# Performance work log

Measured on AMD Instinct MI355X. Metric: run time of the kernel, lower is better.

## Reference

```python
import jax, jax.numpy as jnp
import numpy as np

N_NODES = 50000
N_EDGES = 600000
IN_FEATS = 128
HIDDEN = 256
OUT_FEATS = 64


def setup_inputs() -> dict:
    key = jax.random.key(0)
    ks = jax.random.split(key, 12)
    inv = lambda n: 1.0 / np.sqrt(n)
    return {
        "x": jax.random.normal(ks[0], (N_NODES, IN_FEATS), dtype=jnp.float32),
        "edge_index": jax.random.randint(ks[1], (2, N_EDGES), 0, N_NODES, dtype=jnp.int64),
        "W_sage": jax.random.normal(ks[2], (IN_FEATS, IN_FEATS), dtype=jnp.float32) * inv(IN_FEATS),
        "W1a": jax.random.normal(ks[3], (IN_FEATS, HIDDEN), dtype=jnp.float32) * inv(IN_FEATS),
        "b1a": jax.random.normal(ks[4], (HIDDEN,), dtype=jnp.float32) * 0.01,
        "W1b": jax.random.normal(ks[5], (HIDDEN, OUT_FEATS), dtype=jnp.float32) * inv(HIDDEN),
        "b1b": jax.random.normal(ks[6], (OUT_FEATS,), dtype=jnp.float32) * 0.01,
        "W2a": jax.random.normal(ks[7], (IN_FEATS, HIDDEN), dtype=jnp.float32) * inv(IN_FEATS),
        "b2a": jax.random.normal(ks[8], (HIDDEN,), dtype=jnp.float32) * 0.01,
        "W2b": jax.random.normal(ks[9], (HIDDEN, OUT_FEATS), dtype=jnp.float32) * inv(HIDDEN),
        "b2b": jax.random.normal(ks[10], (OUT_FEATS,), dtype=jnp.float32) * 0.01,
    }


def reference(x, edge_index, W_sage, W1a, b1a, W1b, b1b, W2a, b2a, W2b, b2b):
    n = x.shape[0]
    src, dst = edge_index[0], edge_index[1]
    # SAGEConv mean aggregation: mean over incoming neighbor (source) features at each target node
    summed = jax.ops.segment_sum(x[src], dst, num_segments=n)          # [N, in]
    deg = jax.ops.segment_sum(jnp.ones_like(src, dtype=x.dtype), dst, num_segments=n)
    mean = summed / jnp.maximum(deg, 1.0)[:, None]                     # nodes w/o neighbors -> 0
    x_1hop = mean @ W_sage                                             # lin_l, no root, no bias
    # dual MLP branches (dropout is identity in eval mode)
    out1 = jax.nn.relu(x @ W1a + b1a) @ W1b + b1b
    out2 = jax.nn.relu(x_1hop @ W2a + b2a) @ W2b + b2b
    return out1 + out2
```

## Files before the change

### kernel.cpp

```cpp
#include <hip/hip_runtime.h>

#define N_NODES 50000
#define N_PAD   50048
#define N_EDGES 600000
#define IN_F 128
#define HID 256
#define OUT_F 64
#define ROWS 16
#define SLOTS 56
#define NBLK (N_PAD / ROWS)
#define EPT 4

typedef __attribute__((ext_vector_type(8))) short bf16x8;
typedef __attribute__((ext_vector_type(4))) float f32x4;

__device__ inline short f2bf(float f) {
    unsigned u = __builtin_bit_cast(unsigned, f);
    u += 0x7fffu + ((u >> 16) & 1u);
    return (short)(u >> 16);
}
__device__ inline float bflo(unsigned u) { return __builtin_bit_cast(float, u << 16); }
__device__ inline float bfhi(unsigned u) { return __builtin_bit_cast(float, u & 0xffff0000u); }

__global__ __launch_bounds__(256) void build_kernel(
    const int* __restrict__ ei, int* __restrict__ cursor,
    unsigned short* __restrict__ esrc)
{
    int t0 = blockIdx.x * (256 * EPT) + threadIdx.x;
    int src[EPT], dst[EPT], p[EPT];
    bool v[EPT];
    #pragma unroll
    for (int i = 0; i < EPT; ++i) {
        int e = t0 + i * 256;
        v[i] = e < N_EDGES;
        int ee = v[i] ? e : 0;
        src[i] = ei[ee];
        dst[i] = ei[N_EDGES + ee];
    }
    #pragma unroll
    for (int i = 0; i < EPT; ++i)
        p[i] = v[i] ? atomicAdd(&cursor[dst[i]], 1) : SLOTS;
    #pragma unroll
    for (int i = 0; i < EPT; ++i)
        if (v[i] && p[i] < SLOTS)
            esrc[(size_t)dst[i] * SLOTS + p[i]] = (unsigned short)src[i];
}

__global__ __launch_bounds__(256) void prep_kernel(
    const float* __restrict__ x, short* __restrict__ xb,
    const float* __restrict__ Wsg, const float* __restrict__ W2a,
    const float* __restrict__ W1a, const float* __restrict__ W1b,
    const float* __restrict__ W2b,
    short* __restrict__ F1a, short* __restrict__ F1b,
    short* __restrict__ Fc,  short* __restrict__ F2b)
{
    const int bid = blockIdx.x, t = threadIdx.x;
    if (bid < 3125) {
        int i = bid * 256 + t;
        float4 a0 = *reinterpret_cast<const float4*>(x + (size_t)i * 8);
        float4 a1 = *reinterpret_cast<const float4*>(x + (size_t)i * 8 + 4);
        bf16x8 v;
        v[0] = f2bf(a0.x); v[1] = f2bf(a0.y); v[2] = f2bf(a0.z); v[3] = f2bf(a0.w);
        v[4] = f2bf(a1.x); v[5] = f2bf(a1.y); v[6] = f2bf(a1.z); v[7] = f2bf(a1.w);
        *reinterpret_cast<bf16x8*>(xb + (size_t)i * 8) = v;
        return;
    }
    int cid = (bid - 3125) * 256 + t;
    if (cid >= 6144 && cid < 10240) {
        int c = cid - 6144;
        int lane = c & 63, rem = c >> 6;
        int ks = rem & 3, nt = rem >> 2;
        int col = nt * 16 + (lane & 15);
        int k0 = ks * 32 + (lane >> 4) * 8;
        float acc[8] = {0.f, 0.f, 0.f, 0.f, 0.f, 0.f, 0.f, 0.f};
        for (int m0 = 0; m0 < 128; m0 += 8) {
            float wcol[8];
            #pragma unroll
            for (int mm = 0; mm < 8; ++mm)
                wcol[mm] = W2a[(size_t)(m0 + mm) * HID + col];
            #pragma unroll
            for (int j = 0; j < 8; ++j) {
                #pragma unroll
                for (int mm = 0; mm < 8; ++mm)
                    acc[j] = fmaf(Wsg[(size_t)(k0 + j) * IN_F + m0 + mm], wcol[mm], acc[j]);
            }
        }
        bf16x8 v;
        #pragma unroll
        for (int j = 0; j < 8; ++j) v[j] = f2bf(acc[j]);
        *reinterpret_cast<bf16x8*>(Fc + (size_t)c * 8) = v;
    } else {
        const float* src; short* dst; int N, KST, base;
        if      (cid < 4096)  { src = W1a; dst = F1a; N = 256; KST = 4; base = 0; }
        else if (cid < 6144)  { src = W1b; dst = F1b; N = 64;  KST = 8; base = 4096; }
        else                  { src = W2b; dst = F2b; N = 64;  KST = 8; base = 10240; }
        int c = cid - base;
        int lane = c & 63;
        int rem = c >> 6;
        int ks = rem % KST;
        int nt = rem / KST;
        int col = nt * 16 + (lane & 15);
        int k0 = ks * 32 + (lane >> 4) * 8;
        bf16x8 v;
        #pragma unroll
        for (int j = 0; j < 8; ++j)
            v[j] = f2bf(src[(size_t)(k0 + j) * N + col]);
        *reinterpret_cast<bf16x8*>(dst + (size_t)c * 8) = v;
    }
}

__device__ inline bf16x8 afrag_lds128(const short* S, int lane, int ks) {
    int row = lane & 15, g = lane >> 4;
    int chunk = (ks * 4 + g) ^ row;
    return *reinterpret_cast<const bf16x8*>(
        reinterpret_cast<const char*>(S) + row * 256 + chunk * 16);
}
__device__ inline bf16x8 afrag_lds256(const short* S, int lane, int ks) {
    int row = lane & 15, g = lane >> 4;
    int chunk = (ks * 4 + g) ^ row;
    return *reinterpret_cast<const bf16x8*>(
        reinterpret_cast<const char*>(S) + row * 512 + chunk * 16);
}

__device__ inline void stage1_relu(const bf16x8 afr[4], short* Hs,
                                   const short* __restrict__ Waf,
                                   const float* __restrict__ ba,
                                   int w, int lane)
{
    const int row16 = lane & 15, g = lane >> 4;
    #pragma unroll
    for (int i = 0; i < 4; ++i) {
        int nt = w * 4 + i;
        f32x4 acc = {0.f, 0.f, 0.f, 0.f};
        __builtin_amdgcn_s_setprio(1);
        #pragma unroll
        for (int ks = 0; ks < 4; ++ks) {
            bf16x8 b = *reinterpret_cast<const bf16x8*>(
                Waf + ((size_t)(nt * 4 + ks) * 64 + lane) * 8);
            acc = __builtin_amdgcn_mfma_f32_16x16x32_bf16(afr[ks], b, acc, 0, 0, 0);
        }
        __builtin_amdgcn_s_setprio(0);
        int col = nt * 16 + row16;
        float bias = ba[col];
        #pragma unroll
        for (int reg = 0; reg < 4; ++reg) {
            int hrow = g * 4 + reg;
            float v = fmaxf(acc[reg] + bias, 0.0f);
            *reinterpret_cast<short*>(reinterpret_cast<char*>(Hs)
                + hrow * 512 + ((((col >> 3) ^ hrow) & 31) * 16) + (col & 7) * 2) = f2bf(v);
        }
    }
}

__device__ inline f32x4 stage2_acc(const short* Hs, const short* __restrict__ Wbf,
                                   int w, int lane, f32x4 acc)
{
    __builtin_amdgcn_s_setprio(1);
    #pragma unroll
    for (int ks = 0; ks < 8; ++ks) {
        bf16x8 a = afrag_lds256(Hs, lane, ks);
        bf16x8 b = *reinterpret_cast<const bf16x8*>(
            Wbf + ((size_t)(w * 8 + ks) * 64 + lane) * 8);
        acc = __builtin_amdgcn_mfma_f32_16x16x32_bf16(a, b, acc, 0, 0, 0);
    }
    __builtin_amdgcn_s_setprio(0);
    return acc;
}

__global__ __launch_bounds__(256) void fused_kernel(
    const short* __restrict__ xb, const unsigned short* __restrict__ esrc,
    const int* __restrict__ deg,
    const short* __restrict__ F1a, const float* __restrict__ b1a,
    const short* __restrict__ F1b, const float* __restrict__ b1b,
    const short* __restrict__ Fc,  const float* __restrict__ b2a,
    const short* __restrict__ F2b, const float* __restrict__ b2b,
    float* __restrict__ out)
{
    __shared__ short Ms[16 * 128];
    __shared__ short Hs[16 * 256];
    const int t = threadIdx.x, w = t >> 6, lane = t & 63;
    const long r0 = (long)blockIdx.x * ROWS;
    const int row16 = lane & 15, g = lane >> 4;

    #pragma unroll
    for (int nn = 0; nn < 4; ++nn) {
        int row = w * 4 + nn;
        long node = r0 + row;
        int d = deg[node]; d = min(d, SLOTS);
        int slot = min(lane, SLOTS - 1);
        int my = esrc[(size_t)node * SLOTS + slot];
        float ax = 0.f, ay = 0.f;
        for (int j = 0; j < d; j += 16) {
            unsigned u[16];
            #pragma unroll
            for (int k = 0; k < 16; ++k) {
                int cidx = min(j + k, d - 1);
                int s = __builtin_amdgcn_readlane(my, cidx);
                u[k] = *reinterpret_cast<const unsigned*>(xb + (size_t)s * IN_F + lane * 2);
            }
            #pragma unroll
            for (int k = 0; k < 16; ++k) {
                float wk = (j + k < d) ? 1.0f : 0.0f;
                ax = fmaf(bflo(u[k]), wk, ax);
                ay = fmaf(bfhi(u[k]), wk, ay);
            }
        }
        float inv = (d > 0) ? 1.0f / (float)d : 0.0f;
        ax *= inv; ay *= inv;
        int chunk = (lane >> 2) ^ row;
        unsigned packed = (unsigned)(unsigned short)f2bf(ax)
                        | ((unsigned)(unsigned short)f2bf(ay) << 16);
        *reinterpret_cast<unsigned*>(reinterpret_cast<char*>(Ms)
            + row * 256 + chunk * 16 + (lane & 3) * 4) = packed;
    }
    __syncthreads();

    {
        bf16x8 afr[4];
        #pragma unroll
        for (int ks = 0; ks < 4; ++ks) afr[ks] = afrag_lds128(Ms, lane, ks);
        stage1_relu(afr, Hs, Fc, b2a, w, lane);
    }
    __syncthreads();

    f32x4 oacc = {0.f, 0.f, 0.f, 0.f};
    oacc = stage2_acc(Hs, F2b, w, lane, oacc);
    __syncthreads();

    {
        bf16x8 afr[4];
        const short* xrow = xb + (size_t)(r0 + row16) * IN_F + g * 8;
        #pragma unroll
        for (int ks = 0; ks < 4; ++ks)
            afr[ks] = *reinterpret_cast<const bf16x8*>(xrow + ks * 32);
        stage1_relu(afr, Hs, F1a, b1a, w, lane);
    }
    __syncthreads();

    oacc = stage2_acc(Hs, F1b, w, lane, oacc);
    {
        int col = w * 16 + row16;
        float bias = b1b[col] + b2b[col];
        #pragma unroll
        for (int reg = 0; reg < 4; ++reg) {
            long row = r0 + g * 4 + reg;
            if (row < N_NODES)
                out[row * OUT_F + col] = oacc[reg] + bias;
        }
    }
}

extern "C" void kernel_launch(void* const* d_in, const int* in_sizes, int n_in,
                              void* d_out, int out_size, void* d_ws, size_t ws_size,
                              hipStream_t stream)
{
    const float* x   = (const float*)d_in[0];
    const int*   ei  = (const int*)d_in[1];
    const float* Wsg = (const float*)d_in[2];
    const float* W1a = (const float*)d_in[3];
    const float* b1a = (const float*)d_in[4];
    const float* W1b = (const float*)d_in[5];
    const float* b1b = (const float*)d_in[6];
    const float* W2a = (const float*)d_in[7];
    const float* b2a = (const float*)d_in[8];
    const float* W2b = (const float*)d_in[9];
    const float* b2b = (const float*)d_in[10];
    float* out = (float*)d_out;

    int* cursor = (int*)d_ws;
    unsigned short* esrc = (unsigned short*)(cursor + N_PAD);
    short* F1a = (short*)(esrc + (size_t)N_PAD * SLOTS);
    short* F1b = F1a + 4096 * 8;
    short* Fc  = F1b + 2048 * 8;
    short* F2b = Fc + 4096 * 8;
    short* xb  = F2b + 2048 * 8;

    hipMemsetAsync(cursor, 0, N_PAD * sizeof(int), stream);
    build_kernel<<<(N_EDGES + 256 * EPT - 1) / (256 * EPT), 256, 0, stream>>>(
        ei, cursor, esrc);
    prep_kernel<<<3173, 256, 0, stream>>>(x, xb, Wsg, W2a, W1a, W1b, W2b,
                                          F1a, F1b, Fc, F2b);
    fused_kernel<<<NBLK, 256, 0, stream>>>(xb, esrc, cursor,
                                           F1a, b1a, F1b, b1b,
                                           Fc, b2a, F2b, b2b, out);
}
```

Before: 122.0 us.

## Fold cursor zeroing into prep kernel and gather two nodes per wave iteration

Replaces the hipMemsetAsync on the degree cursor with extra blocks in the prep kernel, removing one launch. The build kernel goes back to one edge per thread. The aggregation loop now processes two nodes at once so more independent gathers are in flight per wave. The s_setprio hints around the MFMA loops are removed. Pairing nodes runs both to the larger degree, which wastes loads when degrees differ, and it raises register pressure.

```diff
diff --git a/kernel.cpp b/kernel.cpp
--- a/kernel.cpp
+++ b/kernel.cpp
@@ -9,7 +9,6 @@
 #define ROWS 16
 #define SLOTS 56
 #define NBLK (N_PAD / ROWS)
-#define EPT 4
 
 typedef __attribute__((ext_vector_type(8))) short bf16x8;
 typedef __attribute__((ext_vector_type(4))) float f32x4;
@@ -21,30 +20,6 @@
 }
 __device__ inline float bflo(unsigned u) { return __builtin_bit_cast(float, u << 16); }
 __device__ inline float bfhi(unsigned u) { return __builtin_bit_cast(float, u & 0xffff0000u); }
-
-__global__ __launch_bounds__(256) void build_kernel(
-    const int* __restrict__ ei, int* __restrict__ cursor,
-    unsigned short* __restrict__ esrc)
-{
-    int t0 = blockIdx.x * (256 * EPT) + threadIdx.x;
-    int src[EPT], dst[EPT], p[EPT];
-    bool v[EPT];
-    #pragma unroll
-    for (int i = 0; i < EPT; ++i) {
-        int e = t0 + i * 256;
-        v[i] = e < N_EDGES;
-        int ee = v[i] ? e : 0;
-        src[i] = ei[ee];
-        dst[i] = ei[N_EDGES + ee];
-    }
-    #pragma unroll
-    for (int i = 0; i < EPT; ++i)
-        p[i] = v[i] ? atomicAdd(&cursor[dst[i]], 1) : SLOTS;
-    #pragma unroll
-    for (int i = 0; i < EPT; ++i)
-        if (v[i] && p[i] < SLOTS)
-            esrc[(size_t)dst[i] * SLOTS + p[i]] = (unsigned short)src[i];
-}
 
 __global__ __launch_bounds__(256) void prep_kernel(
     const float* __restrict__ x, short* __restrict__ xb,
@@ -52,7 +27,8 @@
     const float* __restrict__ W1a, const float* __restrict__ W1b,
     const float* __restrict__ W2b,
     short* __restrict__ F1a, short* __restrict__ F1b,
-    short* __restrict__ Fc,  short* __restrict__ F2b)
+    short* __restrict__ Fc,  short* __restrict__ F2b,
+    int* __restrict__ cursor)
 {
     const int bid = blockIdx.x, t = threadIdx.x;
     if (bid < 3125) {
@@ -63,6 +39,11 @@
         v[0] = f2bf(a0.x); v[1] = f2bf(a0.y); v[2] = f2bf(a0.z); v[3] = f2bf(a0.w);
         v[4] = f2bf(a1.x); v[5] = f2bf(a1.y); v[6] = f2bf(a1.z); v[7] = f2bf(a1.w);
         *reinterpret_cast<bf16x8*>(xb + (size_t)i * 8) = v;
+        return;
+    }
+    if (bid >= 3173) {
+        for (int i = (bid - 3173) * 256 + t; i < N_PAD; i += 27 * 256)
+            cursor[i] = 0;
         return;
     }
     int cid = (bid - 3125) * 256 + t;
@@ -109,6 +90,18 @@
     }
 }
 
+__global__ __launch_bounds__(256) void build_kernel(
+    const int* __restrict__ ei, int* __restrict__ cursor,
+    unsigned short* __restrict__ esrc)
+{
+    int e = blockIdx.x * 256 + threadIdx.x;
+    if (e >= N_EDGES) return;
+    int src = ei[e];
+    int dst = ei[N_EDGES + e];
+    int p = atomicAdd(&cursor[dst], 1);
+    if (p < SLOTS) esrc[(size_t)dst * SLOTS + p] = (unsigned short)src;
+}
+
 __device__ inline bf16x8 afrag_lds128(const short* S, int lane, int ks) {
     int row = lane & 15, g = lane >> 4;
     int chunk = (ks * 4 + g) ^ row;
@@ -132,14 +125,12 @@
     for (int i = 0; i < 4; ++i) {
         int nt = w * 4 + i;
         f32x4 acc = {0.f, 0.f, 0.f, 0.f};
-        __builtin_amdgcn_s_setprio(1);
         #pragma unroll
         for (int ks = 0; ks < 4; ++ks) {
             bf16x8 b = *reinterpret_cast<const bf16x8*>(
                 Waf + ((size_t)(nt * 4 + ks) * 64 + lane) * 8);
             acc = __builtin_amdgcn_mfma_f32_16x16x32_bf16(afr[ks], b, acc, 0, 0, 0);
         }
-        __builtin_amdgcn_s_setprio(0);
         int col = nt * 16 + row16;
         float bias = ba[col];
         #pragma unroll
@@ -155,7 +146,6 @@
 __device__ inline f32x4 stage2_acc(const short* Hs, const short* __restrict__ Wbf,
                                    int w, int lane, f32x4 acc)
 {
-    __builtin_amdgcn_s_setprio(1);
     #pragma unroll
     for (int ks = 0; ks < 8; ++ks) {
         bf16x8 a = afrag_lds256(Hs, lane, ks);
@@ -163,7 +153,6 @@
             Wbf + ((size_t)(w * 8 + ks) * 64 + lane) * 8);
         acc = __builtin_amdgcn_mfma_f32_16x16x32_bf16(a, b, acc, 0, 0, 0);
     }
-    __builtin_amdgcn_s_setprio(0);
     return acc;
 }
 
@@ -182,36 +171,56 @@
     const long r0 = (long)blockIdx.x * ROWS;
     const int row16 = lane & 15, g = lane >> 4;
 
-    #pragma unroll
-    for (int nn = 0; nn < 4; ++nn) {
-        int row = w * 4 + nn;
-        long node = r0 + row;
-        int d = deg[node]; d = min(d, SLOTS);
+    #pragma unroll 1
+    for (int p = 0; p < 2; ++p) {
+        int rowA = w * 4 + p * 2;
+        int rowB = rowA + 1;
+        long nodeA = r0 + rowA, nodeB = r0 + rowB;
+        int dA = min(deg[nodeA], SLOTS);
+        int dB = min(deg[nodeB], SLOTS);
         int slot = min(lane, SLOTS - 1);
-        int my = esrc[(size_t)node * SLOTS + slot];
-        float ax = 0.f, ay = 0.f;
-        for (int j = 0; j < d; j += 16) {
-            unsigned u[16];
-            #pragma unroll
-            for (int k = 0; k < 16; ++k) {
-                int cidx = min(j + k, d - 1);
-                int s = __builtin_amdgcn_readlane(my, cidx);
-                u[k] = *reinterpret_cast<const unsigned*>(xb + (size_t)s * IN_F + lane * 2);
-            }
-            #pragma unroll
-            for (int k = 0; k < 16; ++k) {
-                float wk = (j + k < d) ? 1.0f : 0.0f;
-                ax = fmaf(bflo(u[k]), wk, ax);
-                ay = fmaf(bfhi(u[k]), wk, ay);
-            }
-        }
-        float inv = (d > 0) ? 1.0f / (float)d : 0.0f;
-        ax *= inv; ay *= inv;
-        int chunk = (lane >> 2) ^ row;
-        unsigned packed = (unsigned)(unsigned short)f2bf(ax)
-                        | ((unsigned)(unsigned short)f2bf(ay) << 16);
+        int myA = esrc[(size_t)nodeA * SLOTS + slot];
+        int myB = esrc[(size_t)nodeB * SLOTS + slot];
+        int cA = max(dA - 1, 0), cB = max(dB - 1, 0);
+        int dmax = max(dA, dB);
+        float axA = 0.f, ayA = 0.f, axB = 0.f, ayB = 0.f;
+        for (int j = 0; j < dmax; j += 16) {
+            unsigned ua[16], ub[16];
+            #pragma unroll
+            for (int k = 0; k < 16; ++k) {
+                int s = __builtin_amdgcn_readlane(myA, min(j + k, cA));
+                ua[k] = *reinterpret_cast<const unsigned*>(xb + (size_t)s * IN_F + lane * 2);
+            }
+            #pragma unroll
+            for (int k = 0; k < 16; ++k) {
+                int s = __builtin_amdgcn_readlane(myB, min(j + k, cB));
+                ub[k] = *reinterpret_cast<const unsigned*>(xb + (size_t)s * IN_F + lane * 2);
+            }
+            #pragma unroll
+            for (int k = 0; k < 16; ++k) {
+                float wk = (j + k < dA) ? 1.0f : 0.0f;
+                axA = fmaf(bflo(ua[k]), wk, axA);
+                ayA = fmaf(bfhi(ua[k]), wk, ayA);
+            }
+            #pragma unroll
+            for (int k = 0; k < 16; ++k) {
+                float wk = (j + k < dB) ? 1.0f : 0.0f;
+                axB = fmaf(bflo(ub[k]), wk, axB);
+                ayB = fmaf(bfhi(ub[k]), wk, ayB);
+            }
+        }
+        float invA = (dA > 0) ? 1.0f / (float)dA : 0.0f;
+        float invB = (dB > 0) ? 1.0f / (float)dB : 0.0f;
+        unsigned pkA = (unsigned)(unsigned short)f2bf(axA * invA)
+                     | ((unsigned)(unsigned short)f2bf(ayA * invA) << 16);
+        unsigned pkB = (unsigned)(unsigned short)f2bf(axB * invB)
+                     | ((unsigned)(unsigned short)f2bf(ayB * invB) << 16);
+        int chA = (lane >> 2) ^ rowA;
+        int chB = (lane >> 2) ^ rowB;
         *reinterpret_cast<unsigned*>(reinterpret_cast<char*>(Ms)
-            + row * 256 + chunk * 16 + (lane & 3) * 4) = packed;
+            + rowA * 256 + chA * 16 + (lane & 3) * 4) = pkA;
+        *reinterpret_cast<unsigned*>(reinterpret_cast<char*>(Ms)
+            + rowB * 256 + chB * 16 + (lane & 3) * 4) = pkB;
     }
     __syncthreads();
 
@@ -275,11 +284,9 @@
     short* F2b = Fc + 4096 * 8;
     short* xb  = F2b + 2048 * 8;
 
-    hipMemsetAsync(cursor, 0, N_PAD * sizeof(int), stream);
-    build_kernel<<<(N_EDGES + 256 * EPT - 1) / (256 * EPT), 256, 0, stream>>>(
-        ei, cursor, esrc);
-    prep_kernel<<<3173, 256, 0, stream>>>(x, xb, Wsg, W2a, W1a, W1b, W2b,
-                                          F1a, F1b, Fc, F2b);
+    prep_kernel<<<3200, 256, 0, stream>>>(x, xb, Wsg, W2a, W1a, W1b, W2b,
+                                          F1a, F1b, Fc, F2b, cursor);
+    build_kernel<<<(N_EDGES + 255) / 256, 256, 0, stream>>>(ei, cursor, esrc);
     fused_kernel<<<NBLK, 256, 0, stream>>>(xb, esrc, cursor,
                                            F1a, b1a, F1b, b1b,
                                            Fc, b2a, F2b, b2b, out);
```

Result: faster. 115.0 us (-5.8%).
